# Kernel optimization log

Hardware: AMD Instinct MI355X
Metric: run time of the kernel (lower is better)

The kernel has to match this reference:

```python
import jax, jax.numpy as jnp
import numpy as np

D_MODEL = 512
NUM_HEADS = 8
HEAD_DIM = D_MODEL // NUM_HEADS


def setup_inputs() -> dict:
    key = jax.random.key(0)
    ks = jax.random.split(key, 12)
    B, S = 4, 2048
    s = 1.0 / np.sqrt(D_MODEL)  # torch Linear default init scale (uniform bound)
    def lin(k1, k2):
        W = jax.random.uniform(k1, (D_MODEL, D_MODEL), jnp.float32, -s, s)
        b = jax.random.uniform(k2, (D_MODEL,), jnp.float32, -s, s)
        return W, b
    Wq, bq = lin(ks[0], ks[1])
    Wk, bk = lin(ks[2], ks[3])
    Wv, bv = lin(ks[4], ks[5])
    Wo, bo = lin(ks[6], ks[7])
    return {
        "q": jax.random.normal(ks[8], (B, S, D_MODEL), jnp.float32),
        "k": jax.random.normal(ks[9], (B, S, D_MODEL), jnp.float32),
        "v": jax.random.normal(ks[10], (B, S, D_MODEL), jnp.float32),
        "mask": jnp.ones((B, 1, 1, S), jnp.int32),
        "Wq": Wq, "bq": bq, "Wk": Wk, "bk": bk,
        "Wv": Wv, "bv": bv, "Wo": Wo, "bo": bo,
    }


def reference(q, k, v, mask, Wq, bq, Wk, bk, Wv, bv, Wo, bo):
    B, S, _ = q.shape
    scale = np.sqrt(HEAD_DIM).astype(np.float32)
    # projections; torch Linear: x @ W.T + b
    def split_heads(x):  # [B,S,D] -> [B,H,S,hd]
        return x.reshape(B, S, NUM_HEADS, HEAD_DIM).transpose(0, 2, 1, 3)
    Q = split_heads(q @ Wq.T + bq)
    K = split_heads(k @ Wk.T + bk)
    V = split_heads(v @ Wv.T + bv)
    scores = jnp.einsum('bhqd,bhkd->bhqk', Q, K) / scale
    # NOTE: source calls scores.masked_fill(...) non-in-place and discards the
    # result, so the mask has no effect on the math.
    attn = jax.nn.softmax(scores, axis=-1)
    # dropout is identity in eval / deterministic baseline
    out = jnp.einsum('bhqk,bhkd->bhqd', attn, V)
    out = out.transpose(0, 2, 1, 3).reshape(B, S, D_MODEL)
    return out @ Wo.T + bo
```

## Files before the change

### kernel.cpp

```cpp
#include <hip/hip_runtime.h>

#define NB 4
#define NH 8
#define NS 2048
#define ND 512
#define HD 64
#define KVB 64

typedef __attribute__((ext_vector_type(8))) short s16x8;
typedef __attribute__((ext_vector_type(4))) float f32x4;
typedef __attribute__((ext_vector_type(16))) float f32x16;
typedef __attribute__((ext_vector_type(4))) unsigned int u32x4;

#define L2E 1.44269504088896f
#define CSC (0.125f * L2E)

__device__ __forceinline__ unsigned short f2bf(float f) {
  unsigned int u = __builtin_bit_cast(unsigned int, f);
  u += 0x7FFFu + ((u >> 16) & 1u);
  return (unsigned short)(u >> 16);
}
__device__ __forceinline__ unsigned cvtpk_bf16(float lo, float hi) {
  unsigned r;
  asm("v_cvt_pk_bf16_f32 %0, %1, %2" : "=v"(r) : "v"(lo), "v"(hi));
  return r;
}
__device__ __forceinline__ void pl32swap(unsigned& a, unsigned& b) {
  asm("v_permlane32_swap_b32 %0, %1" : "+v"(a), "+v"(b));
}
__device__ __forceinline__ float exp2s(float x) {
  float r;
  asm("v_exp_f32 %0, %1" : "=v"(r) : "v"(x));
  return r;
}
__device__ __forceinline__ void gl_lds16(const void* g, void* l) {
  __builtin_amdgcn_global_load_lds(
      (const __attribute__((address_space(1))) unsigned int*)g,
      (__attribute__((address_space(3))) unsigned int*)l, 16, 0, 0);
}

__global__ __launch_bounds__(256) void convw_kernel(
    const float* __restrict__ Wq, const float* __restrict__ Wk,
    const float* __restrict__ Wv, const float* __restrict__ Wo,
    unsigned short* __restrict__ Wc)
{
  const int bid = blockIdx.x;
  const int m = bid >> 7;
  const float* __restrict__ src = (m == 0) ? Wq : (m == 1) ? Wk : (m == 2) ? Wv : Wo;
  const float sc = (m == 0) ? CSC : 1.0f;
  const int base = (bid & 127) * 2048 + threadIdx.x * 8;
  float4 a = *(const float4*)(src + base);
  float4 b = *(const float4*)(src + base + 4);
  u32x4 o;
  o[0] = cvtpk_bf16(a.x * sc, a.y * sc);
  o[1] = cvtpk_bf16(a.z * sc, a.w * sc);
  o[2] = cvtpk_bf16(b.x * sc, b.y * sc);
  o[3] = cvtpk_bf16(b.z * sc, b.w * sc);
  *(u32x4*)(Wc + (size_t)m * 262144 + base) = o;
}

__global__ __launch_bounds__(256, 2) void proj_kernel(
    const float* __restrict__ qin, const float* __restrict__ kin,
    const float* __restrict__ vin,
    const float* __restrict__ bq, const float* __restrict__ bk,
    const float* __restrict__ bv,
    const unsigned short* __restrict__ Wc,
    unsigned short* __restrict__ Qp, unsigned short* __restrict__ Kp,
    unsigned short* __restrict__ VpT)
{
  __shared__ short sm[32768];
  short* Bs0 = sm + 16384;

  const int o = blockIdx.z * 256 + blockIdx.y * 4 + blockIdx.x;
  const int wg = (o & 7) * 96 + (o >> 3);
  const int z  = wg >> 8;
  const int m_ = (wg & 255) >> 2;
  const int n_ = wg & 3;

  const float* __restrict__ X    = (z == 0) ? qin : (z == 1) ? kin : vin;
  const float* __restrict__ bias = (z == 0) ? bq  : (z == 1) ? bk  : bv;
  const unsigned short* __restrict__ W = Wc + (size_t)z * 262144;

  const int n0 = n_ * 128;
  const int m0 = m_ * 128;
  const int t = threadIdx.x;
  const int lane = t & 63, w = t >> 6;
  const int wrow = (w >> 1) * 64, wcol = (w & 1) * 64;
  const int l15 = lane & 15, l4 = lane >> 4;
  const int grow = lane >> 3, gc = (lane & 7) ^ grow;

  f32x4 acc[4][4];
  const f32x4 z4 = {0.f, 0.f, 0.f, 0.f};
#pragma unroll
  for (int m = 0; m < 4; ++m)
#pragma unroll
    for (int n = 0; n < 4; ++n) acc[m][n] = z4;

#define ADMA(kt)                                                               \
  {                                                                            \
    const float* xb = X + (size_t)(m0 + w * 32) * ND + (kt) * 64;              \
    char* ad = (char*)sm + w * 8192;                                           \
    _Pragma("unroll") for (int j = 0; j < 8; ++j) {                            \
      const int i = j * 64 + lane;                                             \
      const int rw_ = i >> 4, cc = i & 15;                                     \
      gl_lds16(xb + (size_t)rw_ * ND + ((cc ^ (rw_ & 15)) << 2), ad + j * 1024); \
    }                                                                          \
  }
#define BDMA(kt, bufv)                                                         \
  {                                                                            \
    short* bd = Bs0 + (bufv) * 8192 + w * 2048;                                \
    _Pragma("unroll") for (int j = 0; j < 4; ++j) {                            \
      const unsigned short* bs =                                               \
          W + (size_t)(n0 + w * 32 + j * 8 + grow) * ND + (kt) * 64 + gc * 8;  \
      gl_lds16(bs, bd + j * 512);                                              \
    }                                                                          \
  }

  ADMA(0)
  BDMA(0, 0)
  int buf = 0;
  for (int kt = 0; kt < 8; ++kt) {
    __syncthreads();

    s16x8 af2[2][4];
#pragma unroll
    for (int kk = 0; kk < 2; ++kk)
#pragma unroll
      for (int m = 0; m < 4; ++m) {
        const int r = wrow + m * 16 + l15;
        const int cb = kk * 8 + l4 * 2;
        f32x4 lo = *(const f32x4*)((const char*)sm + r * 256 + ((cb ^ (r & 15)) << 4));
        f32x4 hi = *(const f32x4*)((const char*)sm + r * 256 + (((cb + 1) ^ (r & 15)) << 4));
        u32x4 pk;
        pk[0] = cvtpk_bf16(lo[0], lo[1]);
        pk[1] = cvtpk_bf16(lo[2], lo[3]);
        pk[2] = cvtpk_bf16(hi[0], hi[1]);
        pk[3] = cvtpk_bf16(hi[2], hi[3]);
        af2[kk][m] = __builtin_bit_cast(s16x8, pk);
      }
    __syncthreads();

    if (kt < 7) {
      ADMA(kt + 1)
      BDMA(kt + 1, buf ^ 1)
    }
    const char* Bb = (const char*)(Bs0 + buf * 8192);
    __builtin_amdgcn_s_setprio(1);
#pragma unroll
    for (int kk = 0; kk < 2; ++kk) {
      s16x8 bfr[4];
#pragma unroll
      for (int n = 0; n < 4; ++n) {
        const int r = wcol + n * 16 + l15;
        bfr[n] = *(const s16x8*)(Bb + r * 128 + (((kk * 4 + l4) << 4) ^ ((r & 7) << 4)));
      }
#pragma unroll
      for (int m = 0; m < 4; ++m)
#pragma unroll
        for (int n = 0; n < 4; ++n)
          acc[m][n] = __builtin_amdgcn_mfma_f32_16x16x32_bf16(af2[kk][m], bfr[n], acc[m][n], 0, 0, 0);
    }
    __builtin_amdgcn_s_setprio(0);
    buf ^= 1;
  }
#undef ADMA
#undef BDMA

  __syncthreads();
  short* T = sm;
  const int b = m0 >> 11, sb = m0 & 2047;

  if (z != 2) {
    const float bsc = (z == 0) ? CSC : 1.0f;
#pragma unroll
    for (int n = 0; n < 4; ++n) {
      const int cp = wcol + n * 16 + l15;
      const float bb = bias[n0 + cp] * bsc;
#pragma unroll
      for (int m = 0; m < 4; ++m)
#pragma unroll
        for (int r = 0; r < 4; ++r) {
          const int sp = wrow + m * 16 + l4 * 4 + r;
          T[sp * 136 + cp] = (short)f2bf(acc[m][n][r] + bb);
        }
    }
    __syncthreads();
    unsigned short* P = (z == 0) ? Qp : Kp;
#pragma unroll
    for (int i = 0; i < 8; ++i) {
      const int ch = i * 256 + t;
      const int row = ch >> 4, c = ch & 15;
      const int h = (n0 >> 6) + (c >> 3), dd = (c & 7) * 8;
      s16x8 vv = *(const s16x8*)(T + row * 136 + c * 8);
      *(s16x8*)(P + ((size_t)(b * NH + h) * NS + sb + row) * HD + dd) = vv;
    }
  } else {
#pragma unroll
    for (int n = 0; n < 4; ++n) {
      const int cp = wcol + n * 16 + l15;
      const float bb = bias[n0 + cp];
#pragma unroll
      for (int m = 0; m < 4; ++m) {
        const int sp = wrow + m * 16 + l4 * 4;
        *(unsigned*)(T + cp * 136 + sp)     = cvtpk_bf16(acc[m][n][0] + bb, acc[m][n][1] + bb);
        *(unsigned*)(T + cp * 136 + sp + 2) = cvtpk_bf16(acc[m][n][2] + bb, acc[m][n][3] + bb);
      }
    }
    __syncthreads();
#pragma unroll
    for (int i = 0; i < 8; ++i) {
      const int ch = i * 256 + t;
      const int row = ch >> 4, c = ch & 15;
      s16x8 vv = *(const s16x8*)(T + row * 136 + c * 8);
      *(s16x8*)(VpT + ((size_t)(b * 512 + n0 + row)) * NS + sb + c * 8) = vv;
    }
  }
}

__global__ __launch_bounds__(256, 2) void attn_kernel(
    unsigned short* Qp, const unsigned short* __restrict__ Kp,
    const unsigned short* __restrict__ VpT)
{
  __shared__ short sm[32768];
  short* Ks = sm;
  short* Vs = sm + 16384;

  const int o = blockIdx.y * 16 + blockIdx.x;
  const int wg = (o & 7) * 64 + (o >> 3);
  const int bh = wg >> 4;
  const int q0 = (wg & 15) * 128;

  const int t = threadIdx.x;
  const int lane = t & 63, w = t >> 6;
  const int l31 = lane & 31, hi = lane >> 5;
  const int swz = (l31 & 7) << 4;

  const unsigned short* Qbase = Qp + ((size_t)bh * NS + q0 + w * 32) * HD;
  const unsigned short* Kbase = Kp + (size_t)bh * NS * HD;
  const unsigned short* Vbase = VpT + (size_t)bh * HD * NS;

  s16x8 qf[4];
#pragma unroll
  for (int kf = 0; kf < 4; ++kf)
    qf[kf] = *(const s16x8*)(Qbase + l31 * HD + kf * 16 + hi * 8);

  const int srow = lane >> 3;
  const int scol = (lane & 7) ^ srow;
  const unsigned short* ksrc0 = Kbase + (size_t)(w * 16 + srow) * HD + scol * 8;
  const unsigned short* vsrc0 = Vbase + (size_t)(w * 16 + srow) * NS + scol * 8;

  float lrun = 0.f;
  f32x16 acc[2];
#pragma unroll
  for (int n = 0; n < 2; ++n)
#pragma unroll
    for (int r = 0; r < 16; ++r) acc[n][r] = 0.f;

#define STAGE(p, bufv)                                                         \
  {                                                                            \
    _Pragma("unroll") for (int u = 0; u < 2; ++u) {                            \
      const int tt = 2 * (p) + u;                                              \
      const unsigned short* kp_ = ksrc0 + (size_t)tt * KVB * HD;               \
      const unsigned short* vp_ = vsrc0 + tt * KVB;                            \
      short* kd = Ks + (bufv) * 8192 + u * 4096 + w * 1024;                    \
      short* vd = Vs + (bufv) * 8192 + u * 4096 + w * 1024;                    \
      gl_lds16(kp_, kd);                                                       \
      gl_lds16(kp_ + 8 * HD, kd + 512);                                        \
      gl_lds16(vp_, vd);                                                       \
      gl_lds16(vp_ + 8 * NS, vd + 512);                                        \
    }                                                                          \
  }

  STAGE(0, 0)
  int buf = 0;
  for (int p = 0; p < 16; ++p) {
    __syncthreads();
    if (p < 15) STAGE(p + 1, buf ^ 1)

    const char* Kb = (const char*)(Ks + buf * 8192);
    const char* Vb = (const char*)(Vs + buf * 8192);

    f32x16 sA[2], sB[2];
#pragma unroll
    for (int t2 = 0; t2 < 2; ++t2)
#pragma unroll
      for (int r = 0; r < 16; ++r) { sA[t2][r] = 0.f; sB[t2][r] = 0.f; }

    __builtin_amdgcn_s_setprio(1);
#pragma unroll
    for (int t2 = 0; t2 < 2; ++t2)
#pragma unroll
      for (int kf = 0; kf < 4; ++kf) {
        s16x8 ka = *(const s16x8*)(Kb + (t2 * 32 + l31) * 128 +
                                   (((kf * 2 + hi) << 4) ^ swz));
        sA[t2] = __builtin_amdgcn_mfma_f32_32x32x16_bf16(ka, qf[kf], sA[t2], 0, 0, 0);
      }
#pragma unroll
    for (int t2 = 0; t2 < 2; ++t2)
#pragma unroll
      for (int kf = 0; kf < 4; ++kf) {
        s16x8 kb = *(const s16x8*)(Kb + 8192 + (t2 * 32 + l31) * 128 +
                                   (((kf * 2 + hi) << 4) ^ swz));
        sB[t2] = __builtin_amdgcn_mfma_f32_32x32x16_bf16(kb, qf[kf], sB[t2], 0, 0, 0);
      }
    __builtin_amdgcn_s_setprio(0);

    float pvA[32], pvB[32];
#pragma unroll
    for (int t2 = 0; t2 < 2; ++t2)
#pragma unroll
      for (int r = 0; r < 16; ++r) pvA[t2 * 16 + r] = exp2s(sA[t2][r]);

    s16x8 pafA[4];
#pragma unroll
    for (int idx = 0; idx < 4; ++idx) {
      const float* pp = &pvA[idx * 8];
      unsigned x0 = cvtpk_bf16(pp[0], pp[1]);
      unsigned y0 = cvtpk_bf16(pp[4], pp[5]);
      unsigned x1 = cvtpk_bf16(pp[2], pp[3]);
      unsigned y1 = cvtpk_bf16(pp[6], pp[7]);
      pl32swap(x0, y0);
      pl32swap(x1, y1);
      u32x4 fw = {x0, x1, y0, y1};
      pafA[idx] = __builtin_bit_cast(s16x8, fw);
    }
    __builtin_amdgcn_s_setprio(1);
#pragma unroll
    for (int n = 0; n < 2; ++n)
#pragma unroll
      for (int idx = 0; idx < 4; ++idx) {
        s16x8 va = *(const s16x8*)(Vb + (n * 32 + l31) * 128 +
                                   (((idx * 2 + hi) << 4) ^ swz));
        acc[n] = __builtin_amdgcn_mfma_f32_32x32x16_bf16(va, pafA[idx], acc[n], 0, 0, 0);
      }
    __builtin_amdgcn_s_setprio(0);

#pragma unroll
    for (int t2 = 0; t2 < 2; ++t2)
#pragma unroll
      for (int r = 0; r < 16; ++r) pvB[t2 * 16 + r] = exp2s(sB[t2][r]);

    s16x8 pafB[4];
#pragma unroll
    for (int idx = 0; idx < 4; ++idx) {
      const float* pp = &pvB[idx * 8];
      unsigned x0 = cvtpk_bf16(pp[0], pp[1]);
      unsigned y0 = cvtpk_bf16(pp[4], pp[5]);
      unsigned x1 = cvtpk_bf16(pp[2], pp[3]);
      unsigned y1 = cvtpk_bf16(pp[6], pp[7]);
      pl32swap(x0, y0);
      pl32swap(x1, y1);
      u32x4 fw = {x0, x1, y0, y1};
      pafB[idx] = __builtin_bit_cast(s16x8, fw);
    }
    __builtin_amdgcn_s_setprio(1);
#pragma unroll
    for (int n = 0; n < 2; ++n)
#pragma unroll
      for (int idx = 0; idx < 4; ++idx) {
        s16x8 va = *(const s16x8*)(Vb + 8192 + (n * 32 + l31) * 128 +
                                   (((idx * 2 + hi) << 4) ^ swz));
        acc[n] = __builtin_amdgcn_mfma_f32_32x32x16_bf16(va, pafB[idx], acc[n], 0, 0, 0);
      }
    __builtin_amdgcn_s_setprio(0);

    float s32[32];
#pragma unroll
    for (int i = 0; i < 32; ++i) s32[i] = pvA[i] + pvB[i];
    float s16_[16];
#pragma unroll
    for (int i = 0; i < 16; ++i) s16_[i] = s32[i] + s32[i + 16];
    float s8[8];
#pragma unroll
    for (int i = 0; i < 8; ++i) s8[i] = s16_[i] + s16_[i + 8];
    float s4[4];
#pragma unroll
    for (int i = 0; i < 4; ++i) s4[i] = s8[i] + s8[i + 4];
    float psum = (s4[0] + s4[1]) + (s4[2] + s4[3]);
    lrun += psum + __shfl_xor(psum, 32);

    buf ^= 1;
  }
#undef STAGE

  __syncthreads();
  short* Od = sm;
  const float rinv = 1.0f / lrun;
  const int rw = w * 32 + l31;
#pragma unroll
  for (int n = 0; n < 2; ++n)
#pragma unroll
    for (int g = 0; g < 4; ++g) {
      unsigned lo  = cvtpk_bf16(acc[n][g * 4 + 0] * rinv, acc[n][g * 4 + 1] * rinv);
      unsigned hi2 = cvtpk_bf16(acc[n][g * 4 + 2] * rinv, acc[n][g * 4 + 3] * rinv);
      const int dby = (n * 64 + g * 16 + hi * 8) ^ swz;
      *(unsigned*)((char*)Od + rw * 128 + dby)       = lo;
      *(unsigned*)((char*)Od + rw * 128 + (dby ^ 4)) = hi2;
    }
  __syncthreads();

#pragma unroll
  for (int j = 0; j < 4; ++j) {
    const int ch = j * 256 + t;
    const int q = ch >> 3, c = ch & 7;
    s16x8 vdat = *(const s16x8*)((const char*)Od + q * 128 + ((c ^ (q & 7)) << 4));
    *(s16x8*)(Qp + ((size_t)bh * NS + q0 + q) * HD + c * 8) = vdat;
  }
}

__global__ __launch_bounds__(256) void oproj_kernel(
    const unsigned short* __restrict__ Op, const unsigned short* __restrict__ Wc,
    const float* __restrict__ bo, float* __restrict__ out)
{
  __shared__ short sm[32768];
  short* A0 = sm;
  short* B0 = sm + 16384;

  const int o = blockIdx.y * 4 + blockIdx.x;
  const int wg = (o & 7) * 32 + (o >> 3);
  const int n0 = (wg & 3) * 128;
  const int m0 = (wg >> 2) * 128;
  const int b = m0 >> 11, sb = m0 & 2047;
  const int t = threadIdx.x;
  const int lane = t & 63, w = t >> 6;
  const int wrow = (w >> 1) * 64, wcol = (w & 1) * 64;
  const int l15 = lane & 15, l4 = lane >> 4;
  const int grow = lane >> 3, gc = (lane & 7) ^ grow;
  const unsigned short* Wo16 = Wc + 3 * 262144;

  f32x4 acc[4][4];
  const f32x4 z4 = {0.f, 0.f, 0.f, 0.f};
#pragma unroll
  for (int m = 0; m < 4; ++m)
#pragma unroll
    for (int n = 0; n < 4; ++n) acc[m][n] = z4;

#define ODMA(kt, bufv)                                                         \
  {                                                                            \
    short* ad = A0 + (bufv) * 8192 + w * 2048;                                 \
    short* bd = B0 + (bufv) * 8192 + w * 2048;                                 \
    _Pragma("unroll") for (int j = 0; j < 4; ++j) {                            \
      const unsigned short* as =                                               \
          Op + ((size_t)(b * NH + (kt)) * NS + sb + w * 32 + j * 8 + grow) * HD + gc * 8; \
      gl_lds16(as, ad + j * 512);                                              \
      const unsigned short* bs =                                               \
          Wo16 + (size_t)(n0 + w * 32 + j * 8 + grow) * ND + (kt) * 64 + gc * 8; \
      gl_lds16(bs, bd + j * 512);                                              \
    }                                                                          \
  }

  ODMA(0, 0)
  int buf = 0;
  for (int kt = 0; kt < 8; ++kt) {
    __syncthreads();
    if (kt < 7) ODMA(kt + 1, buf ^ 1)
    const char* Ab = (const char*)(A0 + buf * 8192);
    const char* Bb = (const char*)(B0 + buf * 8192);
    __builtin_amdgcn_s_setprio(1);
#pragma unroll
    for (int kk = 0; kk < 2; ++kk) {
      s16x8 af[4], bfr[4];
#pragma unroll
      for (int m = 0; m < 4; ++m) {
        const int r = wrow + m * 16 + l15;
        af[m] = *(const s16x8*)(Ab + r * 128 + (((kk * 4 + l4) << 4) ^ ((r & 7) << 4)));
      }
#pragma unroll
      for (int n = 0; n < 4; ++n) {
        const int r = wcol + n * 16 + l15;
        bfr[n] = *(const s16x8*)(Bb + r * 128 + (((kk * 4 + l4) << 4) ^ ((r & 7) << 4)));
      }
#pragma unroll
      for (int m = 0; m < 4; ++m)
#pragma unroll
        for (int n = 0; n < 4; ++n)
          acc[m][n] = __builtin_amdgcn_mfma_f32_16x16x32_bf16(af[m], bfr[n], acc[m][n], 0, 0, 0);
    }
    __builtin_amdgcn_s_setprio(0);
    buf ^= 1;
  }
#undef ODMA

#pragma unroll
  for (int n = 0; n < 4; ++n) {
    const int col = n0 + wcol + n * 16 + l15;
    const float bb = bo[col];
#pragma unroll
    for (int m = 0; m < 4; ++m)
#pragma unroll
      for (int r = 0; r < 4; ++r) {
        const int mg = m0 + wrow + m * 16 + l4 * 4 + r;
        out[(size_t)mg * ND + col] = acc[m][n][r] + bb;
      }
  }
}

extern "C" void kernel_launch(void* const* d_in, const int* in_sizes, int n_in,
                              void* d_out, int out_size, void* d_ws, size_t ws_size,
                              hipStream_t stream) {
  const float* q  = (const float*)d_in[0];
  const float* k  = (const float*)d_in[1];
  const float* v  = (const float*)d_in[2];
  const float* Wq = (const float*)d_in[4];
  const float* bq = (const float*)d_in[5];
  const float* Wk = (const float*)d_in[6];
  const float* bk = (const float*)d_in[7];
  const float* Wv = (const float*)d_in[8];
  const float* bv = (const float*)d_in[9];
  const float* Wo = (const float*)d_in[10];
  const float* bo = (const float*)d_in[11];
  float* out = (float*)d_out;

  const size_t headElems = (size_t)NB * NH * NS * HD;
  unsigned short* Qp  = (unsigned short*)d_ws;
  unsigned short* Kp  = Qp + headElems;
  unsigned short* VpT = Kp + headElems;
  unsigned short* Wc  = VpT + headElems;

  hipLaunchKernelGGL(convw_kernel, dim3(512), dim3(256), 0, stream,
                     Wq, Wk, Wv, Wo, Wc);
  hipLaunchKernelGGL(proj_kernel, dim3(4, 64, 3), dim3(256), 0, stream,
                     q, k, v, bq, bk, bv, Wc, Qp, Kp, VpT);
  hipLaunchKernelGGL(attn_kernel, dim3(16, 32), dim3(256), 0, stream,
                     Qp, Kp, VpT);
  hipLaunchKernelGGL(oproj_kernel, dim3(4, 64), dim3(256), 0, stream,
                     Qp, Wc, bo, out);
}
```

Measured before the change: 188.2 us.

## Process two 32-row query blocks per wave to reuse K/V fragments

Each wave now owns 64 query rows instead of 32, so a workgroup covers 256 queries and the grid is halved. Each K fragment read from LDS feeds QK^T MFMAs for both query blocks, and each V fragment feeds both PV accumulations. This cuts LDS reads and global K/V staging per query. In exchange it doubles accumulator and score register usage, relaxes launch bounds to one block per CU, and leaves fewer resident waves and workgroups to hide latency.

Measured after the change: 193.7 us. 1.03x slower.

```diff
diff --git a/kernel.cpp b/kernel.cpp
--- a/kernel.cpp
+++ b/kernel.cpp
@@ -217,7 +217,7 @@
   }
 }
 
-__global__ __launch_bounds__(256, 2) void attn_kernel(
+__global__ __launch_bounds__(256, 1) void attn_kernel(
     unsigned short* Qp, const unsigned short* __restrict__ Kp,
     const unsigned short* __restrict__ VpT)
 {
@@ -225,36 +225,41 @@
   short* Ks = sm;
   short* Vs = sm + 16384;
 
-  const int o = blockIdx.y * 16 + blockIdx.x;
-  const int wg = (o & 7) * 64 + (o >> 3);
-  const int bh = wg >> 4;
-  const int q0 = (wg & 15) * 128;
+  const int o = blockIdx.y * 8 + blockIdx.x;
+  const int wg = (o & 7) * 32 + (o >> 3);
+  const int bh = wg >> 3;
+  const int q0 = (wg & 7) * 256;
 
   const int t = threadIdx.x;
   const int lane = t & 63, w = t >> 6;
   const int l31 = lane & 31, hi = lane >> 5;
   const int swz = (l31 & 7) << 4;
 
-  const unsigned short* Qbase = Qp + ((size_t)bh * NS + q0 + w * 32) * HD;
+  const unsigned short* Qbase = Qp + ((size_t)bh * NS + q0 + w * 64) * HD;
   const unsigned short* Kbase = Kp + (size_t)bh * NS * HD;
   const unsigned short* Vbase = VpT + (size_t)bh * HD * NS;
 
-  s16x8 qf[4];
-#pragma unroll
-  for (int kf = 0; kf < 4; ++kf)
-    qf[kf] = *(const s16x8*)(Qbase + l31 * HD + kf * 16 + hi * 8);
+  s16x8 qf[2][4];
+#pragma unroll
+  for (int qb = 0; qb < 2; ++qb)
+#pragma unroll
+    for (int kf = 0; kf < 4; ++kf)
+      qf[qb][kf] = *(const s16x8*)(Qbase + (qb * 32 + l31) * HD + kf * 16 + hi * 8);
 
   const int srow = lane >> 3;
   const int scol = (lane & 7) ^ srow;
   const unsigned short* ksrc0 = Kbase + (size_t)(w * 16 + srow) * HD + scol * 8;
   const unsigned short* vsrc0 = Vbase + (size_t)(w * 16 + srow) * NS + scol * 8;
 
-  float lrun = 0.f;
-  f32x16 acc[2];
-#pragma unroll
-  for (int n = 0; n < 2; ++n)
-#pragma unroll
-    for (int r = 0; r < 16; ++r) acc[n][r] = 0.f;
+  float lrun[2] = {0.f, 0.f};
+  f32x16 acc[2][2];
+  f32x16 z16;
+#pragma unroll
+  for (int r = 0; r < 16; ++r) z16[r] = 0.f;
+#pragma unroll
+  for (int qb = 0; qb < 2; ++qb)
+#pragma unroll
+    for (int n = 0; n < 2; ++n) acc[qb][n] = z16;
 
 #define STAGE(p, bufv)                                                         \
   {                                                                            \
@@ -277,130 +282,104 @@
     __syncthreads();
     if (p < 15) STAGE(p + 1, buf ^ 1)
 
-    const char* Kb = (const char*)(Ks + buf * 8192);
-    const char* Vb = (const char*)(Vs + buf * 8192);
-
-    f32x16 sA[2], sB[2];
-#pragma unroll
-    for (int t2 = 0; t2 < 2; ++t2)
-#pragma unroll
-      for (int r = 0; r < 16; ++r) { sA[t2][r] = 0.f; sB[t2][r] = 0.f; }
-
-    __builtin_amdgcn_s_setprio(1);
-#pragma unroll
-    for (int t2 = 0; t2 < 2; ++t2)
-#pragma unroll
-      for (int kf = 0; kf < 4; ++kf) {
-        s16x8 ka = *(const s16x8*)(Kb + (t2 * 32 + l31) * 128 +
-                                   (((kf * 2 + hi) << 4) ^ swz));
-        sA[t2] = __builtin_amdgcn_mfma_f32_32x32x16_bf16(ka, qf[kf], sA[t2], 0, 0, 0);
-      }
-#pragma unroll
-    for (int t2 = 0; t2 < 2; ++t2)
-#pragma unroll
-      for (int kf = 0; kf < 4; ++kf) {
-        s16x8 kb = *(const s16x8*)(Kb + 8192 + (t2 * 32 + l31) * 128 +
-                                   (((kf * 2 + hi) << 4) ^ swz));
-        sB[t2] = __builtin_amdgcn_mfma_f32_32x32x16_bf16(kb, qf[kf], sB[t2], 0, 0, 0);
-      }
-    __builtin_amdgcn_s_setprio(0);
-
-    float pvA[32], pvB[32];
-#pragma unroll
-    for (int t2 = 0; t2 < 2; ++t2)
-#pragma unroll
-      for (int r = 0; r < 16; ++r) pvA[t2 * 16 + r] = exp2s(sA[t2][r]);
-
-    s16x8 pafA[4];
-#pragma unroll
-    for (int idx = 0; idx < 4; ++idx) {
-      const float* pp = &pvA[idx * 8];
-      unsigned x0 = cvtpk_bf16(pp[0], pp[1]);
-      unsigned y0 = cvtpk_bf16(pp[4], pp[5]);
-      unsigned x1 = cvtpk_bf16(pp[2], pp[3]);
-      unsigned y1 = cvtpk_bf16(pp[6], pp[7]);
-      pl32swap(x0, y0);
-      pl32swap(x1, y1);
-      u32x4 fw = {x0, x1, y0, y1};
-      pafA[idx] = __builtin_bit_cast(s16x8, fw);
-    }
-    __builtin_amdgcn_s_setprio(1);
-#pragma unroll
-    for (int n = 0; n < 2; ++n)
-#pragma unroll
-      for (int idx = 0; idx < 4; ++idx) {
-        s16x8 va = *(const s16x8*)(Vb + (n * 32 + l31) * 128 +
-                                   (((idx * 2 + hi) << 4) ^ swz));
-        acc[n] = __builtin_amdgcn_mfma_f32_32x32x16_bf16(va, pafA[idx], acc[n], 0, 0, 0);
-      }
-    __builtin_amdgcn_s_setprio(0);
-
-#pragma unroll
-    for (int t2 = 0; t2 < 2; ++t2)
-#pragma unroll
-      for (int r = 0; r < 16; ++r) pvB[t2 * 16 + r] = exp2s(sB[t2][r]);
-
-    s16x8 pafB[4];
-#pragma unroll
-    for (int idx = 0; idx < 4; ++idx) {
-      const float* pp = &pvB[idx * 8];
-      unsigned x0 = cvtpk_bf16(pp[0], pp[1]);
-      unsigned y0 = cvtpk_bf16(pp[4], pp[5]);
-      unsigned x1 = cvtpk_bf16(pp[2], pp[3]);
-      unsigned y1 = cvtpk_bf16(pp[6], pp[7]);
-      pl32swap(x0, y0);
-      pl32swap(x1, y1);
-      u32x4 fw = {x0, x1, y0, y1};
-      pafB[idx] = __builtin_bit_cast(s16x8, fw);
-    }
-    __builtin_amdgcn_s_setprio(1);
-#pragma unroll
-    for (int n = 0; n < 2; ++n)
-#pragma unroll
-      for (int idx = 0; idx < 4; ++idx) {
-        s16x8 va = *(const s16x8*)(Vb + 8192 + (n * 32 + l31) * 128 +
-                                   (((idx * 2 + hi) << 4) ^ swz));
-        acc[n] = __builtin_amdgcn_mfma_f32_32x32x16_bf16(va, pafB[idx], acc[n], 0, 0, 0);
-      }
-    __builtin_amdgcn_s_setprio(0);
-
-    float s32[32];
-#pragma unroll
-    for (int i = 0; i < 32; ++i) s32[i] = pvA[i] + pvB[i];
-    float s16_[16];
-#pragma unroll
-    for (int i = 0; i < 16; ++i) s16_[i] = s32[i] + s32[i + 16];
-    float s8[8];
-#pragma unroll
-    for (int i = 0; i < 8; ++i) s8[i] = s16_[i] + s16_[i + 8];
-    float s4[4];
-#pragma unroll
-    for (int i = 0; i < 4; ++i) s4[i] = s8[i] + s8[i + 4];
-    float psum = (s4[0] + s4[1]) + (s4[2] + s4[3]);
-    lrun += psum + __shfl_xor(psum, 32);
-
+#pragma unroll
+    for (int sub = 0; sub < 2; ++sub) {
+      const char* Kb = (const char*)(Ks + buf * 8192 + sub * 4096);
+      const char* Vb = (const char*)(Vs + buf * 8192 + sub * 4096);
+
+      s16x8 ka[2][4];
+#pragma unroll
+      for (int t2 = 0; t2 < 2; ++t2)
+#pragma unroll
+        for (int kf = 0; kf < 4; ++kf)
+          ka[t2][kf] = *(const s16x8*)(Kb + (t2 * 32 + l31) * 128 +
+                                       (((kf * 2 + hi) << 4) ^ swz));
+
+      f32x16 sacc[2][2];
+      __builtin_amdgcn_s_setprio(1);
+#pragma unroll
+      for (int qb = 0; qb < 2; ++qb)
+#pragma unroll
+        for (int t2 = 0; t2 < 2; ++t2) {
+          sacc[qb][t2] = __builtin_amdgcn_mfma_f32_32x32x16_bf16(ka[t2][0], qf[qb][0], z16, 0, 0, 0);
+#pragma unroll
+          for (int kf = 1; kf < 4; ++kf)
+            sacc[qb][t2] = __builtin_amdgcn_mfma_f32_32x32x16_bf16(ka[t2][kf], qf[qb][kf], sacc[qb][t2], 0, 0, 0);
+        }
+      __builtin_amdgcn_s_setprio(0);
+
+      s16x8 paf[2][4];
+#pragma unroll
+      for (int qb = 0; qb < 2; ++qb) {
+        float pv[32];
+#pragma unroll
+        for (int t2 = 0; t2 < 2; ++t2)
+#pragma unroll
+          for (int r = 0; r < 16; ++r) pv[t2 * 16 + r] = exp2s(sacc[qb][t2][r]);
+
+        float s16_[16];
+#pragma unroll
+        for (int i = 0; i < 16; ++i) s16_[i] = pv[i] + pv[i + 16];
+        float s8[8];
+#pragma unroll
+        for (int i = 0; i < 8; ++i) s8[i] = s16_[i] + s16_[i + 8];
+        float s4[4];
+#pragma unroll
+        for (int i = 0; i < 4; ++i) s4[i] = s8[i] + s8[i + 4];
+        float psum = (s4[0] + s4[1]) + (s4[2] + s4[3]);
+        lrun[qb] += psum + __shfl_xor(psum, 32);
+
+#pragma unroll
+        for (int idx = 0; idx < 4; ++idx) {
+          const float* pp = &pv[idx * 8];
+          unsigned x0 = cvtpk_bf16(pp[0], pp[1]);
+          unsigned y0 = cvtpk_bf16(pp[4], pp[5]);
+          unsigned x1 = cvtpk_bf16(pp[2], pp[3]);
+          unsigned y1 = cvtpk_bf16(pp[6], pp[7]);
+          pl32swap(x0, y0);
+          pl32swap(x1, y1);
+          u32x4 fw = {x0, x1, y0, y1};
+          paf[qb][idx] = __builtin_bit_cast(s16x8, fw);
+        }
+      }
+
+      __builtin_amdgcn_s_setprio(1);
+#pragma unroll
+      for (int n = 0; n < 2; ++n)
+#pragma unroll
+        for (int idx = 0; idx < 4; ++idx) {
+          s16x8 va = *(const s16x8*)(Vb + (n * 32 + l31) * 128 +
+                                     (((idx * 2 + hi) << 4) ^ swz));
+          acc[0][n] = __builtin_amdgcn_mfma_f32_32x32x16_bf16(va, paf[0][idx], acc[0][n], 0, 0, 0);
+          acc[1][n] = __builtin_amdgcn_mfma_f32_32x32x16_bf16(va, paf[1][idx], acc[1][n], 0, 0, 0);
+        }
+      __builtin_amdgcn_s_setprio(0);
+    }
     buf ^= 1;
   }
 #undef STAGE
 
   __syncthreads();
   short* Od = sm;
-  const float rinv = 1.0f / lrun;
-  const int rw = w * 32 + l31;
-#pragma unroll
-  for (int n = 0; n < 2; ++n)
-#pragma unroll
-    for (int g = 0; g < 4; ++g) {
-      unsigned lo  = cvtpk_bf16(acc[n][g * 4 + 0] * rinv, acc[n][g * 4 + 1] * rinv);
-      unsigned hi2 = cvtpk_bf16(acc[n][g * 4 + 2] * rinv, acc[n][g * 4 + 3] * rinv);
-      const int dby = (n * 64 + g * 16 + hi * 8) ^ swz;
-      *(unsigned*)((char*)Od + rw * 128 + dby)       = lo;
-      *(unsigned*)((char*)Od + rw * 128 + (dby ^ 4)) = hi2;
-    }
+#pragma unroll
+  for (int qb = 0; qb < 2; ++qb) {
+    const float rinv = 1.0f / lrun[qb];
+    const int rw = w * 64 + qb * 32 + l31;
+#pragma unroll
+    for (int n = 0; n < 2; ++n)
+#pragma unroll
+      for (int g = 0; g < 4; ++g) {
+        unsigned lo  = cvtpk_bf16(acc[qb][n][g * 4 + 0] * rinv, acc[qb][n][g * 4 + 1] * rinv);
+        unsigned hi2 = cvtpk_bf16(acc[qb][n][g * 4 + 2] * rinv, acc[qb][n][g * 4 + 3] * rinv);
+        const int dby = (n * 64 + g * 16 + hi * 8) ^ swz;
+        *(unsigned*)((char*)Od + rw * 128 + dby)       = lo;
+        *(unsigned*)((char*)Od + rw * 128 + (dby ^ 4)) = hi2;
+      }
+  }
   __syncthreads();
 
 #pragma unroll
-  for (int j = 0; j < 4; ++j) {
+  for (int j = 0; j < 8; ++j) {
     const int ch = j * 256 + t;
     const int q = ch >> 3, c = ch & 7;
     s16x8 vdat = *(const s16x8*)((const char*)Od + q * 128 + ((c ^ (q & 7)) << 4));
@@ -521,7 +500,7 @@
                      Wq, Wk, Wv, Wo, Wc);
   hipLaunchKernelGGL(proj_kernel, dim3(4, 64, 3), dim3(256), 0, stream,
                      q, k, v, bq, bk, bv, Wc, Qp, Kp, VpT);
-  hipLaunchKernelGGL(attn_kernel, dim3(16, 32), dim3(256), 0, stream,
+  hipLaunchKernelGGL(attn_kernel, dim3(8, 32), dim3(256), 0, stream,
                      Qp, Kp, VpT);
   hipLaunchKernelGGL(oproj_kernel, dim3(4, 64), dim3(256), 0, stream,
                      Qp, Wc, bo, out);
```
